# Kernel tuning notes

Measured on AMD Instinct MI355X. Metric: run time of the kernel, lower is better.

## Reference

```python
import jax, jax.numpy as jnp
import numpy as np

B, N, IN_DIM, HID, OUT, HEADS = 2, 1024, 64, 64, 64, 4
PHD1, PHD2 = HID // HEADS, OUT // HEADS
SLOPE = 0.2  # PyG GATv2Conv default negative_slope
EPS = 1e-12  # F.normalize eps


def _gatv2_dense(x, Wl, Wr, att, bias, heads, phd, mask):
    """Dense GATv2 layer over a full adjacency mask.
    x: [B,N,Din]; Wl/Wr: [Din, heads*phd]; att: [heads,phd]; bias: [heads*phd];
    mask: [N,N] bool, mask[i,j]=True means edge j->i exists.
    """
    Bb, Nn, _ = x.shape
    xl = (x @ Wl).reshape(Bb, Nn, heads, phd)  # source features
    xr = (x @ Wr).reshape(Bb, Nn, heads, phd)  # target features
    # s[b,i,j,h,p] = leaky_relu(xr[b,i] + xl[b,j])  (GATv2)
    s = jax.nn.leaky_relu(xr[:, :, None] + xl[:, None, :], SLOPE)
    e = jnp.einsum('bijhp,hp->bijh', s, att)  # [B,Ni,Nj,H]
    e = jnp.where(mask[None, :, :, None], e, -jnp.inf)
    alpha = jax.nn.softmax(e, axis=2)  # softmax over source nodes j
    out = jnp.einsum('bijh,bjhp->bihp', alpha, xl).reshape(Bb, Nn, heads * phd)
    return out + bias


def setup_inputs() -> dict:
    key = jax.random.key(0)
    ks = jax.random.split(key, 10)
    sc = 0.1
    return {
        'x': jax.random.normal(ks[0], (B, N, IN_DIM), jnp.float32),
        'embedding': jax.random.normal(ks[1], (N, HID), jnp.float32),
        'Wl1': jax.random.normal(ks[2], (IN_DIM, HEADS * PHD1), jnp.float32) * sc,
        'Wr1': jax.random.normal(ks[3], (IN_DIM, HEADS * PHD1), jnp.float32) * sc,
        'att1': jax.random.normal(ks[4], (HEADS, PHD1), jnp.float32) * sc,
        'b1': jnp.zeros((HEADS * PHD1,), jnp.float32),
        'Wl2': jax.random.normal(ks[5], (HID, HEADS * PHD2), jnp.float32) * sc,
        'Wr2': jax.random.normal(ks[6], (HID, HEADS * PHD2), jnp.float32) * sc,
        'att2': jax.random.normal(ks[7], (HEADS, PHD2), jnp.float32) * sc,
        'b2': jnp.zeros((HEADS * PHD2,), jnp.float32),
    }


def reference(x, embedding, Wl1, Wr1, att1, b1, Wl2, Wr2, att2, b2):
    # AdaptiveAdjacency: cosine-similarity adjacency; only its nonzero pattern is used.
    norm = jnp.maximum(jnp.linalg.norm(embedding, axis=1, keepdims=True), EPS)
    ne = embedding / norm
    adj = ne @ ne.T  # [N,N]
    # edge set = adj.nonzero(); GATv2Conv(add_self_loops=True) guarantees diagonal
    mask = (adj != 0) | jnp.eye(N, dtype=bool)
    h = jax.nn.relu(_gatv2_dense(x, Wl1, Wr1, att1, b1, HEADS, PHD1, mask))
    # dropout(0.3) in eval mode -> identity
    return _gatv2_dense(h, Wl2, Wr2, att2, b2, HEADS, PHD2, mask)
```

## Files before the change

kernel.cpp:

```cpp
#include <hip/hip_runtime.h>
#include <math.h>

#define NN 1024
#define LOG2E 1.4426950408889634f

template <int CTRL>
__device__ __forceinline__ float dpp_mov(float x) {
    int xi = __builtin_bit_cast(int, x);
    int r = __builtin_amdgcn_update_dpp(0, xi, CTRL, 0xF, 0xF, true);
    return __builtin_bit_cast(float, r);
}
__device__ __forceinline__ float dpp_rowsum16(float t) {
    t += dpp_mov<0x111>(t);
    t += dpp_mov<0x112>(t);
    t += dpp_mov<0x114>(t);
    t += dpp_mov<0x118>(t);
    return t;
}
__device__ __forceinline__ float quad_sum4(float t) {
    t += dpp_mov<0xB1>(t);
    t += dpp_mov<0x4E>(t);
    return t;
}

__device__ void mask_tile(const float* __restrict__ emb,
                          unsigned char* __restrict__ mask, int task, float* sm) {
    float* As = sm;
    float* Bs = sm + 32 * 65;
    int tid = threadIdx.x;
    int ib = (task & 31) << 5;
    int jb = (task >> 5) << 4;
    #pragma unroll
    for (int r = 0; r < 2; ++r) {
        int q = tid + (r << 8);
        int row = q >> 4, c4 = (q & 15) << 2;
        float4 a = *(const float4*)&emb[(ib + row) * 64 + c4];
        As[row * 65 + c4 + 0] = a.x; As[row * 65 + c4 + 1] = a.y;
        As[row * 65 + c4 + 2] = a.z; As[row * 65 + c4 + 3] = a.w;
    }
    {
        int row = tid >> 4, c4 = (tid & 15) << 2;
        float4 b = *(const float4*)&emb[(jb + row) * 64 + c4];
        Bs[row * 65 + c4 + 0] = b.x; Bs[row * 65 + c4 + 1] = b.y;
        Bs[row * 65 + c4 + 2] = b.z; Bs[row * 65 + c4 + 3] = b.w;
    }
    __syncthreads();
    int i1 = tid >> 4, j = tid & 15;
    float acc1 = 0.f, acc2 = 0.f;
    #pragma unroll 8
    for (int k = 0; k < 64; ++k) {
        float bv = Bs[j * 65 + k];
        acc1 = fmaf(As[i1 * 65 + k], bv, acc1);
        acc2 = fmaf(As[(i1 + 16) * 65 + k], bv, acc2);
    }
    int gi1 = ib + i1, gi2 = ib + i1 + 16, gj = jb + j;
    mask[gi1 * NN + gj] = (acc1 != 0.f || gi1 == gj) ? 1 : 0;
    mask[gi2 * NN + gj] = (acc2 != 0.f || gi2 == gj) ? 1 : 0;
}

__device__ void gemm_row(const float* __restrict__ Wl, const float* __restrict__ Wr,
                         const float* __restrict__ att, const float* hrow,
                         float* __restrict__ xl, float* __restrict__ xr,
                         float* __restrict__ alE, int r) {
    int tid = threadIdx.x;
    if (tid < 64) {
        int c = tid;
        float accl = 0.f, accr = 0.f;
        #pragma unroll 8
        for (int p = 0; p < 64; ++p) {
            float a = hrow[p];
            accl = fmaf(a, Wl[p * 64 + c], accl);
            accr = fmaf(a, Wr[p * 64 + c], accr);
        }
        xl[r * 64 + c] = accl;
        xr[r * 64 + c] = accr;
        float t = dpp_rowsum16(accl * att[c]);
        if ((c & 15) == 15) alE[(r << 2) | (c >> 4)] = 0.6f * LOG2E * t;
    }
}

__device__ void attn_partial(const float* __restrict__ xl, const float* __restrict__ xr,
                             const float* __restrict__ att, const float* __restrict__ alE,
                             const unsigned char* __restrict__ mask,
                             float* __restrict__ Opar, float* __restrict__ lpar,
                             int task, float* sm) {
    float* sO = sm;
    float* sL = sm + 2048;
    int tid = threadIdx.x;
    int wave = tid >> 6, lane = tid & 63;
    int h = lane & 3, jl = lane >> 2;
    int js = task & 1;
    int p  = task >> 1;
    int b  = p >> 9;
    int i0 = (p & 511) << 1;
    int jbase = (js << 9) + (wave << 7) + (jl << 3);

    const float* xlb = xl + (b << 16);
    float at[16], xr0f[16], xr1f[16];
    {
        const float* ap = att + (h << 2);
        const float* r0 = xr + (((b << 10) + i0) << 6) + (h << 2);
        const float* r1 = r0 + 64;
        #pragma unroll
        for (int q = 0; q < 4; ++q) {
            *(float4*)&at[q << 2]   = *(const float4*)(ap + (q << 4));
            *(float4*)&xr0f[q << 2] = *(const float4*)(r0 + (q << 4));
            *(float4*)&xr1f[q << 2] = *(const float4*)(r1 + (q << 4));
        }
        #pragma unroll
        for (int pp = 0; pp < 16; ++pp) at[pp] *= 0.4f * LOG2E;
    }
    float ar0q[4], ar1q[4];
    #pragma unroll
    for (int q = 0; q < 4; ++q) {
        float p0 = 0.f, p1 = 0.f;
        #pragma unroll
        for (int rr = 0; rr < 4; ++rr) {
            p0 = fmaf(at[(q << 2) + rr], xr0f[(q << 2) + rr], p0);
            p1 = fmaf(at[(q << 2) + rr], xr1f[(q << 2) + rr], p1);
        }
        ar0q[q] = 1.5f * quad_sum4(p0);
        ar1q[q] = 1.5f * quad_sum4(p1);
    }
    unsigned mb0 = 0, mb1 = 0;
    {
        const unsigned* m0p = (const unsigned*)(mask + i0 * NN + jbase);
        const unsigned* m1p = (const unsigned*)(mask + (i0 + 1) * NN + jbase);
        #pragma unroll
        for (int q = 0; q < 2; ++q) {
            unsigned w0 = m0p[q], w1 = m1p[q];
            mb0 |= ((((w0 >> 0) & 1) | ((w0 >> 7) & 2) | ((w0 >> 14) & 4) | ((w0 >> 21) & 8)) << (q << 2));
            mb1 |= ((((w1 >> 0) & 1) | ((w1 >> 7) & 2) | ((w1 >> 14) & 4) | ((w1 >> 21) & 8)) << (q << 2));
        }
    }
    float O0[16], O1[16], l0q[4] = {0,0,0,0}, l1q[4] = {0,0,0,0};
    #pragma unroll
    for (int pp = 0; pp < 16; ++pp) { O0[pp] = 0.f; O1[pp] = 0.f; }
    const float* xrow = xlb + (jbase << 6) + (h << 2);
    const float* alp  = alE + (b << 12) + (jbase << 2);
    #pragma unroll 2
    for (int s = 0; s < 8; ++s) {
        const float* rp = xrow + (s << 6);
        float xv[16];
        *(float4*)&xv[0]  = *(const float4*)(rp);
        *(float4*)&xv[4]  = *(const float4*)(rp + 16);
        *(float4*)&xv[8]  = *(const float4*)(rp + 32);
        *(float4*)&xv[12] = *(const float4*)(rp + 48);
        float alr[4];
        *(float4*)alr = *(const float4*)(alp + (s << 2));
        bool m0 = (mb0 >> s) & 1, m1 = (mb1 >> s) & 1;
        #pragma unroll
        for (int q = 0; q < 4; ++q) {
            float p0 = 0.f, p1 = 0.f;
            #pragma unroll
            for (int rr = 0; rr < 4; ++rr) {
                float xvv = xv[(q << 2) + rr];
                float a = at[(q << 2) + rr];
                p0 = fmaf(a, __builtin_fabsf(xr0f[(q << 2) + rr] + xvv), p0);
                p1 = fmaf(a, __builtin_fabsf(xr1f[(q << 2) + rr] + xvv), p1);
            }
            float e0 = quad_sum4(p0) + (ar0q[q] + alr[q]);
            float e1 = quad_sum4(p1) + (ar1q[q] + alr[q]);
            float pe0 = m0 ? __builtin_amdgcn_exp2f(e0) : 0.f;
            float pe1 = m1 ? __builtin_amdgcn_exp2f(e1) : 0.f;
            l0q[q] += pe0; l1q[q] += pe1;
            #pragma unroll
            for (int rr = 0; rr < 4; ++rr) {
                float xvv = xv[(q << 2) + rr];
                O0[(q << 2) + rr] = fmaf(pe0, xvv, O0[(q << 2) + rr]);
                O1[(q << 2) + rr] = fmaf(pe1, xvv, O1[(q << 2) + rr]);
            }
        }
    }
    #pragma unroll
    for (int pp = 0; pp < 16; ++pp) {
        O0[pp] += dpp_mov<0x114>(O0[pp]); O0[pp] += dpp_mov<0x118>(O0[pp]);
        O1[pp] += dpp_mov<0x114>(O1[pp]); O1[pp] += dpp_mov<0x118>(O1[pp]);
    }
    #pragma unroll
    for (int q = 0; q < 4; ++q) {
        l0q[q] += dpp_mov<0x114>(l0q[q]); l0q[q] += dpp_mov<0x118>(l0q[q]);
        l1q[q] += dpp_mov<0x114>(l1q[q]); l1q[q] += dpp_mov<0x118>(l1q[q]);
    }
    if ((lane & 15) >= 12) {
        int k = lane >> 4;
        int wk = (wave << 2) + k;
        #pragma unroll
        for (int q = 0; q < 4; ++q) {
            *(float4*)&sO[(wk)      * 64 + (q << 4) + (h << 2)] = *(const float4*)&O0[q << 2];
            *(float4*)&sO[(16 + wk) * 64 + (q << 4) + (h << 2)] = *(const float4*)&O1[q << 2];
        }
        if (h == 0) {
            #pragma unroll
            for (int q = 0; q < 4; ++q) {
                sL[(wk << 2) + q]      = l0q[q];
                sL[64 + (wk << 2) + q] = l1q[q];
            }
        }
    }
    __syncthreads();
    if (tid < 128) {
        int ii = tid >> 6, c = tid & 63;
        float o = 0.f, l = 0.f;
        #pragma unroll
        for (int wk = 0; wk < 16; ++wk) {
            o += sO[(ii * 16 + wk) * 64 + c];
            l += sL[ii * 64 + (wk << 2) + (c >> 4)];
        }
        int idx = (((p << 1) | ii) << 1) | js;
        Opar[(idx << 6) + c] = o;
        if ((c & 15) == 0) lpar[(idx << 2) + (c >> 4)] = l;
    }
}

__device__ __forceinline__ float combine_val(const float* __restrict__ Opar,
                                             const float* __restrict__ lpar,
                                             const float* __restrict__ bias,
                                             int r, int c) {
    int b = r >> 10, i = r & 1023;
    int p = (b << 9) | (i >> 1);
    int ii = i & 1;
    int base = ((p << 1) | ii) << 1;
    float o = Opar[(base << 6) + c] + Opar[((base + 1) << 6) + c];
    float l = lpar[(base << 2) + (c >> 4)] + lpar[((base + 1) << 2) + (c >> 4)];
    return o / l + bias[c];
}

__global__ __launch_bounds__(256) void k_p1(const float* __restrict__ x,
                                            const float* __restrict__ emb,
                                            const float* __restrict__ Wl1,
                                            const float* __restrict__ Wr1,
                                            const float* __restrict__ att1,
                                            unsigned char* __restrict__ mask,
                                            float* __restrict__ xl,
                                            float* __restrict__ xr,
                                            float* __restrict__ alE) {
    __shared__ float sm[32 * 65 + 16 * 65];
    __shared__ float hrow[64];
    int bid = blockIdx.x;
    if (threadIdx.x < 64) hrow[threadIdx.x] = x[bid * 64 + threadIdx.x];
    mask_tile(emb, mask, bid, sm);
    __syncthreads();
    gemm_row(Wl1, Wr1, att1, hrow, xl, xr, alE, bid);
}

__global__ __launch_bounds__(256) void k_attn_f(const float* __restrict__ xl,
                                                const float* __restrict__ xr,
                                                const float* __restrict__ att,
                                                const float* __restrict__ alE,
                                                const unsigned char* __restrict__ mask,
                                                float* __restrict__ Opar,
                                                float* __restrict__ lpar) {
    __shared__ float sm[2176];
    attn_partial(xl, xr, att, alE, mask, Opar, lpar, blockIdx.x, sm);
}

__global__ __launch_bounds__(256) void k_comb_gemm(const float* __restrict__ Opar,
                                                   const float* __restrict__ lpar,
                                                   const float* __restrict__ b1,
                                                   const float* __restrict__ Wl2,
                                                   const float* __restrict__ Wr2,
                                                   const float* __restrict__ att2,
                                                   float* __restrict__ xl,
                                                   float* __restrict__ xr,
                                                   float* __restrict__ alE) {
    __shared__ float hrow[64];
    int bid = blockIdx.x;
    if (threadIdx.x < 64)
        hrow[threadIdx.x] = fmaxf(combine_val(Opar, lpar, b1, bid, threadIdx.x), 0.f);
    __syncthreads();
    gemm_row(Wl2, Wr2, att2, hrow, xl, xr, alE, bid);
}

__global__ __launch_bounds__(64) void k_comb_out(const float* __restrict__ Opar,
                                                 const float* __restrict__ lpar,
                                                 const float* __restrict__ b2,
                                                 float* __restrict__ out) {
    out[blockIdx.x * 64 + threadIdx.x] =
        combine_val(Opar, lpar, b2, blockIdx.x, threadIdx.x);
}

extern "C" void kernel_launch(void* const* d_in, const int* in_sizes, int n_in,
                              void* d_out, int out_size, void* d_ws, size_t ws_size,
                              hipStream_t stream) {
    const float* x    = (const float*)d_in[0];
    const float* emb  = (const float*)d_in[1];
    const float* Wl1  = (const float*)d_in[2];
    const float* Wr1  = (const float*)d_in[3];
    const float* att1 = (const float*)d_in[4];
    const float* b1   = (const float*)d_in[5];
    const float* Wl2  = (const float*)d_in[6];
    const float* Wr2  = (const float*)d_in[7];
    const float* att2 = (const float*)d_in[8];
    const float* b2   = (const float*)d_in[9];
    float* out = (float*)d_out;

    unsigned char* mask = (unsigned char*)d_ws;
    float* xl   = (float*)(mask + NN * NN);
    float* xr   = xl + 2 * NN * 64;
    float* alE  = xr + 2 * NN * 64;
    float* Opar = alE + 2 * NN * 4;
    float* lpar = Opar + 1024 * 2 * 2 * 64;

    k_p1<<<2048, 256, 0, stream>>>(x, emb, Wl1, Wr1, att1, mask, xl, xr, alE);
    k_attn_f<<<2048, 256, 0, stream>>>(xl, xr, att1, alE, mask, Opar, lpar);
    k_comb_gemm<<<2048, 256, 0, stream>>>(Opar, lpar, b1, Wl2, Wr2, att2, xl, xr, alE);
    k_attn_f<<<2048, 256, 0, stream>>>(xl, xr, att2, alE, mask, Opar, lpar);
    k_comb_out<<<2048, 64, 0, stream>>>(Opar, lpar, b2, out);
}
```

Baseline: 149.2 us.

## Drop split-j attention partials and fuse combine into attention kernels

Each attention block now covers all 1024 source nodes for its pair of target rows, instead of splitting j into two halves and writing partial O/l to global memory. Because of that, the combine, ReLU and layer-2 GEMM are fused into the end of the first attention kernel, and the final normalize plus bias into the second. This cuts the launch count from five to three and removes the Opar/lpar round trips. In exchange the grid is halved to 1024 blocks, each with a longer serial j-loop, and a separate buffer set for layer 2 is added.

Result: no change. 147.7 us (-1.0%).

```diff
diff --git a/kernel.cpp b/kernel.cpp
--- a/kernel.cpp
+++ b/kernel.cpp
@@ -58,42 +58,18 @@
     mask[gi2 * NN + gj] = (acc2 != 0.f || gi2 == gj) ? 1 : 0;
 }
 
-__device__ void gemm_row(const float* __restrict__ Wl, const float* __restrict__ Wr,
-                         const float* __restrict__ att, const float* hrow,
-                         float* __restrict__ xl, float* __restrict__ xr,
-                         float* __restrict__ alE, int r) {
-    int tid = threadIdx.x;
-    if (tid < 64) {
-        int c = tid;
-        float accl = 0.f, accr = 0.f;
-        #pragma unroll 8
-        for (int p = 0; p < 64; ++p) {
-            float a = hrow[p];
-            accl = fmaf(a, Wl[p * 64 + c], accl);
-            accr = fmaf(a, Wr[p * 64 + c], accr);
-        }
-        xl[r * 64 + c] = accl;
-        xr[r * 64 + c] = accr;
-        float t = dpp_rowsum16(accl * att[c]);
-        if ((c & 15) == 15) alE[(r << 2) | (c >> 4)] = 0.6f * LOG2E * t;
-    }
-}
-
-__device__ void attn_partial(const float* __restrict__ xl, const float* __restrict__ xr,
-                             const float* __restrict__ att, const float* __restrict__ alE,
-                             const unsigned char* __restrict__ mask,
-                             float* __restrict__ Opar, float* __restrict__ lpar,
-                             int task, float* sm) {
+__device__ void attn_core(const float* __restrict__ xl, const float* __restrict__ xr,
+                          const float* __restrict__ att, const float* __restrict__ alE,
+                          const unsigned char* __restrict__ mask,
+                          int p, float* sm, float& oOut, float& lOut) {
     float* sO = sm;
     float* sL = sm + 2048;
     int tid = threadIdx.x;
     int wave = tid >> 6, lane = tid & 63;
     int h = lane & 3, jl = lane >> 2;
-    int js = task & 1;
-    int p  = task >> 1;
     int b  = p >> 9;
     int i0 = (p & 511) << 1;
-    int jbase = (js << 9) + (wave << 7) + (jl << 3);
+    int j0 = (wave << 8) + (jl << 4);
 
     const float* xlb = xl + (b << 16);
     float at[16], xr0f[16], xr1f[16];
@@ -124,10 +100,10 @@
     }
     unsigned mb0 = 0, mb1 = 0;
     {
-        const unsigned* m0p = (const unsigned*)(mask + i0 * NN + jbase);
-        const unsigned* m1p = (const unsigned*)(mask + (i0 + 1) * NN + jbase);
-        #pragma unroll
-        for (int q = 0; q < 2; ++q) {
+        const unsigned* m0p = (const unsigned*)(mask + i0 * NN + j0);
+        const unsigned* m1p = (const unsigned*)(mask + (i0 + 1) * NN + j0);
+        #pragma unroll
+        for (int q = 0; q < 4; ++q) {
             unsigned w0 = m0p[q], w1 = m1p[q];
             mb0 |= ((((w0 >> 0) & 1) | ((w0 >> 7) & 2) | ((w0 >> 14) & 4) | ((w0 >> 21) & 8)) << (q << 2));
             mb1 |= ((((w1 >> 0) & 1) | ((w1 >> 7) & 2) | ((w1 >> 14) & 4) | ((w1 >> 21) & 8)) << (q << 2));
@@ -136,10 +112,10 @@
     float O0[16], O1[16], l0q[4] = {0,0,0,0}, l1q[4] = {0,0,0,0};
     #pragma unroll
     for (int pp = 0; pp < 16; ++pp) { O0[pp] = 0.f; O1[pp] = 0.f; }
-    const float* xrow = xlb + (jbase << 6) + (h << 2);
-    const float* alp  = alE + (b << 12) + (jbase << 2);
+    const float* xrow = xlb + (j0 << 6) + (h << 2);
+    const float* alp  = alE + (b << 12) + (j0 << 2);
     #pragma unroll 2
-    for (int s = 0; s < 8; ++s) {
+    for (int s = 0; s < 16; ++s) {
         const float* rp = xrow + (s << 6);
         float xv[16];
         *(float4*)&xv[0]  = *(const float4*)(rp);
@@ -207,23 +183,8 @@
             o += sO[(ii * 16 + wk) * 64 + c];
             l += sL[ii * 64 + (wk << 2) + (c >> 4)];
         }
-        int idx = (((p << 1) | ii) << 1) | js;
-        Opar[(idx << 6) + c] = o;
-        if ((c & 15) == 0) lpar[(idx << 2) + (c >> 4)] = l;
-    }
-}
-
-__device__ __forceinline__ float combine_val(const float* __restrict__ Opar,
-                                             const float* __restrict__ lpar,
-                                             const float* __restrict__ bias,
-                                             int r, int c) {
-    int b = r >> 10, i = r & 1023;
-    int p = (b << 9) | (i >> 1);
-    int ii = i & 1;
-    int base = ((p << 1) | ii) << 1;
-    float o = Opar[(base << 6) + c] + Opar[((base + 1) << 6) + c];
-    float l = lpar[(base << 2) + (c >> 4)] + lpar[((base + 1) << 2) + (c >> 4)];
-    return o / l + bias[c];
+        oOut = o; lOut = l;
+    }
 }
 
 __global__ __launch_bounds__(256) void k_p1(const float* __restrict__ x,
@@ -238,46 +199,77 @@
     __shared__ float sm[32 * 65 + 16 * 65];
     __shared__ float hrow[64];
     int bid = blockIdx.x;
-    if (threadIdx.x < 64) hrow[threadIdx.x] = x[bid * 64 + threadIdx.x];
+    int tid = threadIdx.x;
+    if (tid < 64) hrow[tid] = x[bid * 64 + tid];
     mask_tile(emb, mask, bid, sm);
     __syncthreads();
-    gemm_row(Wl1, Wr1, att1, hrow, xl, xr, alE, bid);
-}
-
-__global__ __launch_bounds__(256) void k_attn_f(const float* __restrict__ xl,
-                                                const float* __restrict__ xr,
-                                                const float* __restrict__ att,
-                                                const float* __restrict__ alE,
-                                                const unsigned char* __restrict__ mask,
-                                                float* __restrict__ Opar,
-                                                float* __restrict__ lpar) {
+    if (tid < 64) {
+        int c = tid;
+        float accl = 0.f, accr = 0.f;
+        #pragma unroll 8
+        for (int p = 0; p < 64; ++p) {
+            float a = hrow[p];
+            accl = fmaf(a, Wl1[p * 64 + c], accl);
+            accr = fmaf(a, Wr1[p * 64 + c], accr);
+        }
+        xl[bid * 64 + c] = accl;
+        xr[bid * 64 + c] = accr;
+        float t = dpp_rowsum16(accl * att1[c]);
+        if ((c & 15) == 15) alE[(bid << 2) | (c >> 4)] = 0.6f * LOG2E * t;
+    }
+}
+
+__global__ __launch_bounds__(256, 4) void k_attn_gemm(
+    const float* __restrict__ xl1, const float* __restrict__ xr1,
+    const float* __restrict__ att1, const float* __restrict__ alE1,
+    const unsigned char* __restrict__ mask, const float* __restrict__ b1,
+    const float* __restrict__ Wl2, const float* __restrict__ Wr2,
+    const float* __restrict__ att2,
+    float* __restrict__ xl2, float* __restrict__ xr2, float* __restrict__ alE2)
+{
     __shared__ float sm[2176];
-    attn_partial(xl, xr, att, alE, mask, Opar, lpar, blockIdx.x, sm);
-}
-
-__global__ __launch_bounds__(256) void k_comb_gemm(const float* __restrict__ Opar,
-                                                   const float* __restrict__ lpar,
-                                                   const float* __restrict__ b1,
-                                                   const float* __restrict__ Wl2,
-                                                   const float* __restrict__ Wr2,
-                                                   const float* __restrict__ att2,
-                                                   float* __restrict__ xl,
-                                                   float* __restrict__ xr,
-                                                   float* __restrict__ alE) {
-    __shared__ float hrow[64];
-    int bid = blockIdx.x;
-    if (threadIdx.x < 64)
-        hrow[threadIdx.x] = fmaxf(combine_val(Opar, lpar, b1, bid, threadIdx.x), 0.f);
+    __shared__ float hrow[2][64];
+    float o = 0.f, l = 1.f;
+    attn_core(xl1, xr1, att1, alE1, mask, blockIdx.x, sm, o, l);
+    int tid = threadIdx.x;
+    if (tid < 128) {
+        int ii = tid >> 6, c = tid & 63;
+        hrow[ii][c] = fmaxf(o / l + b1[c], 0.f);
+    }
     __syncthreads();
-    gemm_row(Wl2, Wr2, att2, hrow, xl, xr, alE, bid);
-}
-
-__global__ __launch_bounds__(64) void k_comb_out(const float* __restrict__ Opar,
-                                                 const float* __restrict__ lpar,
-                                                 const float* __restrict__ b2,
-                                                 float* __restrict__ out) {
-    out[blockIdx.x * 64 + threadIdx.x] =
-        combine_val(Opar, lpar, b2, blockIdx.x, threadIdx.x);
+    if (tid < 128) {
+        int ii = tid >> 6, c = tid & 63;
+        int g = ((blockIdx.x >> 9) << 10) + ((blockIdx.x & 511) << 1) + ii;
+        const float* hr = hrow[ii];
+        float accl = 0.f, accr = 0.f;
+        #pragma unroll 8
+        for (int p = 0; p < 64; ++p) {
+            float a = hr[p];
+            accl = fmaf(a, Wl2[p * 64 + c], accl);
+            accr = fmaf(a, Wr2[p * 64 + c], accr);
+        }
+        xl2[g * 64 + c] = accl;
+        xr2[g * 64 + c] = accr;
+        float t = dpp_rowsum16(accl * att2[c]);
+        if ((c & 15) == 15) alE2[(g << 2) | (c >> 4)] = 0.6f * LOG2E * t;
+    }
+}
+
+__global__ __launch_bounds__(256, 4) void k_attn_out(
+    const float* __restrict__ xl2, const float* __restrict__ xr2,
+    const float* __restrict__ att2, const float* __restrict__ alE2,
+    const unsigned char* __restrict__ mask, const float* __restrict__ b2,
+    float* __restrict__ out)
+{
+    __shared__ float sm[2176];
+    float o = 0.f, l = 1.f;
+    attn_core(xl2, xr2, att2, alE2, mask, blockIdx.x, sm, o, l);
+    int tid = threadIdx.x;
+    if (tid < 128) {
+        int ii = tid >> 6, c = tid & 63;
+        int g = ((blockIdx.x >> 9) << 10) + ((blockIdx.x & 511) << 1) + ii;
+        out[g * 64 + c] = o / l + b2[c];
+    }
 }
 
 extern "C" void kernel_launch(void* const* d_in, const int* in_sizes, int n_in,
@@ -296,15 +288,15 @@
     float* out = (float*)d_out;
 
     unsigned char* mask = (unsigned char*)d_ws;
-    float* xl   = (float*)(mask + NN * NN);
-    float* xr   = xl + 2 * NN * 64;
-    float* alE  = xr + 2 * NN * 64;
-    float* Opar = alE + 2 * NN * 4;
-    float* lpar = Opar + 1024 * 2 * 2 * 64;
-
-    k_p1<<<2048, 256, 0, stream>>>(x, emb, Wl1, Wr1, att1, mask, xl, xr, alE);
-    k_attn_f<<<2048, 256, 0, stream>>>(xl, xr, att1, alE, mask, Opar, lpar);
-    k_comb_gemm<<<2048, 256, 0, stream>>>(Opar, lpar, b1, Wl2, Wr2, att2, xl, xr, alE);
-    k_attn_f<<<2048, 256, 0, stream>>>(xl, xr, att2, alE, mask, Opar, lpar);
-    k_comb_out<<<2048, 64, 0, stream>>>(Opar, lpar, b2, out);
-}
+    float* xl1  = (float*)(mask + NN * NN);
+    float* xr1  = xl1 + 2 * NN * 64;
+    float* alE1 = xr1 + 2 * NN * 64;
+    float* xl2  = alE1 + 2 * NN * 4;
+    float* xr2  = xl2 + 2 * NN * 64;
+    float* alE2 = xr2 + 2 * NN * 64;
+
+    k_p1<<<2048, 256, 0, stream>>>(x, emb, Wl1, Wr1, att1, mask, xl1, xr1, alE1);
+    k_attn_gemm<<<1024, 256, 0, stream>>>(xl1, xr1, att1, alE1, mask, b1,
+                                          Wl2, Wr2, att2, xl2, xr2, alE2);
+    k_attn_out<<<1024, 256, 0, stream>>>(xl2, xr2, att2, alE2, mask, b2, out);
+}
```
